# Kernel optimization log

Measured on AMD Instinct MI355X. Metric: run time of the kernel, lower is better.

Reference implementation:

```python
import jax, jax.numpy as jnp
import numpy as np
import math

ALPHA = math.exp(-0.001 * 1000.0)  # exp(-dt * tau_filter_inv)
T, B, D_IN, D_OUT = 2048, 32, 512, 512


def setup_inputs() -> dict:
    key = jax.random.key(0)
    k1, k2, k3 = jax.random.split(key, 3)
    bound = 1.0 / math.sqrt(D_IN)  # torch Linear default init range
    return {
        "input_tensor": jax.random.normal(k1, (T, B, D_IN), dtype=jnp.float32),
        "weight": jax.random.uniform(k2, (D_OUT, D_IN), minval=-bound, maxval=bound, dtype=jnp.float32),
        "bias": jax.random.uniform(k3, (D_OUT,), minval=-bound, maxval=bound, dtype=jnp.float32),
    }


def reference(input_tensor, weight, bias):
    # y[t] = W x[t] + b   -> [T, B, D_OUT]
    y = jnp.einsum("tbi,oi->tbo", input_tensor, weight) + bias
    alpha = jnp.asarray(ALPHA, dtype=y.dtype)

    # out[0] = y[0]; out[t] = alpha * out[t-1] + y[t]
    def step(carry, yt):
        out = alpha * carry + yt
        return out, out

    _, rest = jax.lax.scan(step, y[0], y[1:])
    return jnp.concatenate([y[:1], rest], axis=0)
```

## Files before the change

kernel.cpp:

```cpp
#include <hip/hip_runtime.h>
#include <stdint.h>

#define T_DIM 2048
#define B_DIM 32
#define DIN   512
#define DOUT  512
#define M_DIM (T_DIM * B_DIM)
#define COLS  (B_DIM * DIN)
#define COLS4 (COLS / 4)

#define ALPHA_F 0.36787944117144233f
#define INV_1MA 1.5819767068693265f

#define FT_T    32
#define FT_HALO 8
#define FT_ROWS (FT_T + FT_HALO)
#define FT_C4   32
#define FT_TT   (T_DIM / FT_T)
#define FT_CT   (COLS4 / FT_C4)

#define FCHUNKS  32
#define FCHUNK_T 64
#define FHALO    16

typedef float  floatx4 __attribute__((ext_vector_type(4)));
typedef __bf16 bf16x8  __attribute__((ext_vector_type(8)));

__device__ __forceinline__ uint32_t pk2(float a, float b) {
  uint32_t ua = __float_as_uint(a); ua += 0x7fffu + ((ua >> 16) & 1u);
  uint32_t ub = __float_as_uint(b); ub += 0x7fffu + ((ub >> 16) & 1u);
  return (ua >> 16) | (ub & 0xffff0000u);
}

__device__ __forceinline__ void gload_lds16(const void* g, void* lds) {
  __builtin_amdgcn_global_load_lds(
      (const __attribute__((address_space(1))) void*)g,
      (__attribute__((address_space(3))) void*)lds,
      16, 0, 0);
}

__device__ __forceinline__ void fma4(float4& c, const float4& v) {
  c.x = fmaf(ALPHA_F, c.x, v.x);
  c.y = fmaf(ALPHA_F, c.y, v.y);
  c.z = fmaf(ALPHA_F, c.z, v.z);
  c.w = fmaf(ALPHA_F, c.w, v.w);
}

__global__ void filter_x_kernel(const float* __restrict__ X,
                                uint16_t* __restrict__ XF,
                                const float* __restrict__ W,
                                uint16_t* __restrict__ WB)
{
  __shared__ __align__(16) float4 L4[FT_ROWS * FT_C4];

  if (blockIdx.y == FT_TT) {
    const int base = (blockIdx.x * 256 + threadIdx.x) * 8;
    const float4* W4 = (const float4*)W;
    float4 w0 = W4[base / 4];
    float4 w1 = W4[base / 4 + 1];
    uint4 p;
    p.x = pk2(w0.x, w0.y); p.y = pk2(w0.z, w0.w);
    p.z = pk2(w1.x, w1.y); p.w = pk2(w1.z, w1.w);
    *(uint4*)&WB[base] = p;
    return;
  }

  const int ct = blockIdx.x;
  const int tt = blockIdx.y;
  const int tid  = threadIdx.x;
  const int lane = tid & 63;
  const int w    = tid >> 6;
  const int t0   = tt * FT_T;
  const size_t gc4 = (size_t)ct * FT_C4;

  const int lrow = lane >> 5;
  const int lcol = lane & 31;

  if (tt == 0) {
    const float4 z = {0.0f, 0.0f, 0.0f, 0.0f};
    L4[tid] = z;
#pragma unroll
    for (int i = 0; i < 4; ++i) {
      const int row = 8 + (w * 4 + i) * 2;
      gload_lds16(X + ((size_t)(t0 + row - 8 + lrow) * COLS4 + gc4 + lcol) * 4,
                  &L4[row * FT_C4]);
    }
  } else {
#pragma unroll
    for (int i = 0; i < 5; ++i) {
      const int row = (w * 5 + i) * 2;
      gload_lds16(X + ((size_t)(t0 - 8 + row + lrow) * COLS4 + gc4 + lcol) * 4,
                  &L4[row * FT_C4]);
    }
  }
  __syncthreads();

  const int tg  = tid >> 5;
  const int col = tid & 31;
  float4 carry = {0.0f, 0.0f, 0.0f, 0.0f};
#pragma unroll
  for (int j = 0; j < 12; ++j) {
    float4 v = L4[(tg * 4 + j) * FT_C4 + col];
    fma4(carry, v);
    if (j >= 8) {
      const int o = tg * 4 + j - 8;
      uint2 p;
      p.x = pk2(carry.x, carry.y);
      p.y = pk2(carry.z, carry.w);
      *(uint2*)&XF[((size_t)(t0 + o) * COLS4 + gc4 + col) * 4] = p;
    }
  }
}

__launch_bounds__(256, 4)
__global__ void gemm_bf16_kernel(const uint16_t* __restrict__ XF,
                                 const uint16_t* __restrict__ WB,
                                 const float* __restrict__ bias,
                                 float* __restrict__ Y)
{
  __shared__ __align__(16) uint16_t As[128 * 64];
  __shared__ __align__(16) uint16_t Bs[128 * 64];

  const int bid = blockIdx.x;
  const int lg = (bid & 7) * 256 + (bid >> 3);
  const int n0 = (lg & 3) * 128;
  const int m0 = (lg >> 2) * 128;

  const int tid  = threadIdx.x;
  const int lane = tid & 63;
  const int w    = tid >> 6;
  const int r    = lane & 15;
  const int q    = lane >> 4;
  const int wm   = w >> 1;
  const int wn   = w & 1;

  const int srow_base = w * 32 + (lane >> 3);
  const int schunk    = lane & 7;

  floatx4 acc[4][4];
#pragma unroll
  for (int i = 0; i < 4; ++i)
#pragma unroll
    for (int j = 0; j < 4; ++j) {
      floatx4 z = {0.0f, 0.0f, 0.0f, 0.0f};
      acc[i][j] = z;
    }

  for (int kt = 0; kt < DIN / 64; ++kt) {
    const int k0 = kt * 64;
#pragma unroll
    for (int i = 0; i < 4; ++i) {
      const int row = srow_base + i * 8;
      const int sc = schunk ^ (row & 7);
      gload_lds16(XF + (size_t)(m0 + row) * DIN + k0 + sc * 8,
                  &As[(w * 32 + i * 8) * 64]);
      gload_lds16(WB + (size_t)(n0 + row) * DIN + k0 + sc * 8,
                  &Bs[(w * 32 + i * 8) * 64]);
    }
    __syncthreads();

#pragma unroll
    for (int kk = 0; kk < 2; ++kk) {
      bf16x8 af[4], bfr[4];
#pragma unroll
      for (int mi = 0; mi < 4; ++mi) {
        const int row = wm * 64 + mi * 16 + r;
        const int cch = (kk * 4 + q) ^ (row & 7);
        af[mi] = *(const bf16x8*)&As[row * 64 + (cch << 3)];
      }
#pragma unroll
      for (int ni = 0; ni < 4; ++ni) {
        const int row = wn * 64 + ni * 16 + r;
        const int cch = (kk * 4 + q) ^ (row & 7);
        bfr[ni] = *(const bf16x8*)&Bs[row * 64 + (cch << 3)];
      }
#pragma unroll
      for (int mi = 0; mi < 4; ++mi)
#pragma unroll
        for (int ni = 0; ni < 4; ++ni)
          acc[mi][ni] = __builtin_amdgcn_mfma_f32_16x16x32_bf16(
              af[mi], bfr[ni], acc[mi][ni], 0, 0, 0);
    }
    __syncthreads();
  }

#pragma unroll
  for (int mi = 0; mi < 4; ++mi) {
    const int rowb = m0 + wm * 64 + mi * 16;
    const int t = rowb >> 5;
    const float s = (1.0f - __expf(-(float)(t + 1))) * INV_1MA;
#pragma unroll
    for (int ni = 0; ni < 4; ++ni) {
      const int col = n0 + wn * 64 + ni * 16 + r;
      const float sb = s * bias[col];
#pragma unroll
      for (int j = 0; j < 4; ++j)
        Y[(size_t)(rowb + q * 4 + j) * DOUT + col] = acc[mi][ni][j] + sb;
    }
  }
}

__launch_bounds__(256, 2)
__global__ void gemm_bias_kernel(const float* __restrict__ X,
                                 const float* __restrict__ W,
                                 const float* __restrict__ bias,
                                 float* __restrict__ Y,
                                 float* __restrict__ halo,
                                 int halo_on)
{
  __shared__ __align__(16) uint16_t As[128 * 64];
  __shared__ __align__(16) uint16_t Bsh[128 * 64];

  const int tid  = threadIdx.x;
  const int lane = tid & 63;
  const int wave = tid >> 6;
  const int wm   = wave >> 1;
  const int wn   = wave & 1;
  const int r    = lane & 15;
  const int q    = lane >> 4;

  const int m0 = blockIdx.y * 128;
  const int n0 = blockIdx.x * 128;

  floatx4 acc[4][4];
#pragma unroll
  for (int i = 0; i < 4; ++i)
#pragma unroll
    for (int j = 0; j < 4; ++j) {
      floatx4 z = {0.0f, 0.0f, 0.0f, 0.0f};
      acc[i][j] = z;
    }

  for (int kt = 0; kt < DIN / 64; ++kt) {
    const int k0 = kt * 64;
#pragma unroll
    for (int j = 0; j < 4; ++j) {
      const int cid = tid + j * 256;
      const int row = cid >> 3;
      const int c   = cid & 7;
      const int slot = (c ^ (row & 7)) << 3;

      const float* ga = &X[(size_t)(m0 + row) * DIN + k0 + c * 8];
      float4 a0 = *(const float4*)ga;
      float4 a1 = *(const float4*)(ga + 4);
      uint4 pa;
      pa.x = pk2(a0.x, a0.y); pa.y = pk2(a0.z, a0.w);
      pa.z = pk2(a1.x, a1.y); pa.w = pk2(a1.z, a1.w);
      *(uint4*)&As[row * 64 + slot] = pa;

      const float* gb = &W[(size_t)(n0 + row) * DIN + k0 + c * 8];
      float4 b0 = *(const float4*)gb;
      float4 b1 = *(const float4*)(gb + 4);
      uint4 pb;
      pb.x = pk2(b0.x, b0.y); pb.y = pk2(b0.z, b0.w);
      pb.z = pk2(b1.x, b1.y); pb.w = pk2(b1.z, b1.w);
      *(uint4*)&Bsh[row * 64 + slot] = pb;
    }
    __syncthreads();

#pragma unroll
    for (int kk = 0; kk < 2; ++kk) {
      bf16x8 af[4], bfr[4];
#pragma unroll
      for (int mi = 0; mi < 4; ++mi) {
        const int row = wm * 64 + mi * 16 + r;
        const int c   = (kk * 4 + q) ^ (row & 7);
        af[mi] = *(const bf16x8*)&As[row * 64 + (c << 3)];
      }
#pragma unroll
      for (int ni = 0; ni < 4; ++ni) {
        const int row = wn * 64 + ni * 16 + r;
        const int c   = (kk * 4 + q) ^ (row & 7);
        bfr[ni] = *(const bf16x8*)&Bsh[row * 64 + (c << 3)];
      }
#pragma unroll
      for (int mi = 0; mi < 4; ++mi)
#pragma unroll
        for (int ni = 0; ni < 4; ++ni)
          acc[mi][ni] = __builtin_amdgcn_mfma_f32_16x16x32_bf16(
              af[mi], bfr[ni], acc[mi][ni], 0, 0, 0);
    }
    __syncthreads();
  }

#pragma unroll
  for (int ni = 0; ni < 4; ++ni) {
    const int col = n0 + wn * 64 + ni * 16 + r;
    const float bv = bias[col];
#pragma unroll
    for (int mi = 0; mi < 4; ++mi) {
      const int rowm = m0 + wm * 64 + mi * 16 + q * 4;
      const int t = rowm >> 5;
      const int b = rowm & 31;
      const int tloc = t & (FCHUNK_T - 1);
      const bool hw = halo_on && (tloc >= FCHUNK_T - FHALO) && (t < T_DIM - FCHUNK_T);
      const size_t hbase = hw
          ? ((size_t)(((t >> 6) + 1) * FHALO + (tloc - (FCHUNK_T - FHALO))) * COLS)
          : 0;
#pragma unroll
      for (int j = 0; j < 4; ++j) {
        const float v = acc[mi][ni][j] + bv;
        Y[(size_t)(rowm + j) * DOUT + col] = v;
        if (hw) halo[hbase + (size_t)(b + j) * DOUT + col] = v;
      }
    }
  }
}

__global__ void scan_kernel(float* __restrict__ Y,
                            const float* __restrict__ halo,
                            int chunk_len)
{
  const int col4 = blockIdx.x * blockDim.x + threadIdx.x;
  const int c = blockIdx.y;

  float4* Y4 = (float4*)Y;
  const float4* H4 = (const float4*)halo;

  float4 carry = {0.0f, 0.0f, 0.0f, 0.0f};
  if (c > 0) {
#pragma unroll
    for (int h = 0; h < FHALO; ++h) {
      float4 v = H4[(size_t)(c * FHALO + h) * COLS4 + col4];
      fma4(carry, v);
    }
  }

  size_t idx = (size_t)c * chunk_len * COLS4 + col4;
  float4 ynext = Y4[idx];
  for (int t = 0; t < chunk_len; ++t) {
    float4 y = ynext;
    if (t + 1 < chunk_len) ynext = Y4[idx + COLS4];
    fma4(carry, y);
    Y4[idx] = carry;
    idx += COLS4;
  }
}

extern "C" void kernel_launch(void* const* d_in, const int* in_sizes, int n_in,
                              void* d_out, int out_size, void* d_ws, size_t ws_size,
                              hipStream_t stream)
{
  const float* X    = (const float*)d_in[0];
  const float* W    = (const float*)d_in[1];
  const float* bias = (const float*)d_in[2];
  float* Y = (float*)d_out;

  const size_t need_new = (size_t)M_DIM * DIN * 2 + (size_t)DOUT * DIN * 2;

  if (ws_size >= need_new) {
    uint16_t* XF = (uint16_t*)d_ws;
    uint16_t* WB = XF + (size_t)M_DIM * DIN;

    dim3 gf(FT_CT, FT_TT + 1);
    filter_x_kernel<<<gf, 256, 0, stream>>>(X, XF, W, WB);
    gemm_bf16_kernel<<<2048, 256, 0, stream>>>(XF, WB, bias, Y);
  } else {
    float* halo = (float*)d_ws;
    const size_t halo_need = (size_t)FCHUNKS * FHALO * COLS * sizeof(float);
    const int halo_on = (ws_size >= halo_need) ? 1 : 0;

    dim3 g1(DOUT / 128, M_DIM / 128);
    gemm_bias_kernel<<<g1, 256, 0, stream>>>(X, W, bias, Y, halo, halo_on);

    const int n_chunks = halo_on ? FCHUNKS : 1;
    dim3 g2(COLS4 / 256, n_chunks);
    scan_kernel<<<g2, 256, 0, stream>>>(Y, halo, T_DIM / n_chunks);
  }
}
```

Measured before the change: 86.53 us.

## Replace bf16 GEMM with 256x256 tile, 4-stage async LDS pipeline

Swaps the 128x128 single-buffered bf16 GEMM for a 256x256-tile kernel with 512 threads. It uses a 4-deep ring of K=32 LDS buffers filled by global_load_lds, with explicit vmcnt waits and barriers. The aim is to overlap global loads with MFMA work and to raise arithmetic intensity per tile. In exchange it uses more registers (32 accumulators per wave) and launches only 512 blocks, which may leave load imbalance across CUs.

```diff
diff --git a/kernel.cpp b/kernel.cpp
--- a/kernel.cpp
+++ b/kernel.cpp
@@ -19,6 +19,9 @@
 #define FT_TT   (T_DIM / FT_T)
 #define FT_CT   (COLS4 / FT_C4)
 
+#define GBK  32
+#define NKT  (DIN / GBK)
+
 #define FCHUNKS  32
 #define FCHUNK_T 64
 #define FHALO    16
@@ -44,6 +47,16 @@
   c.y = fmaf(ALPHA_F, c.y, v.y);
   c.z = fmaf(ALPHA_F, c.z, v.z);
   c.w = fmaf(ALPHA_F, c.w, v.w);
+}
+
+__device__ __forceinline__ void waitcnt_vm(int n) {
+  switch (n) {
+    case 12: asm volatile("s_waitcnt vmcnt(12)" ::: "memory"); break;
+    case 8:  asm volatile("s_waitcnt vmcnt(8)"  ::: "memory"); break;
+    case 4:  asm volatile("s_waitcnt vmcnt(4)"  ::: "memory"); break;
+    default: asm volatile("s_waitcnt vmcnt(0)"  ::: "memory"); break;
+  }
+  __builtin_amdgcn_sched_barrier(0);
 }
 
 __global__ void filter_x_kernel(const float* __restrict__ X,
@@ -112,81 +125,94 @@
   }
 }
 
-__launch_bounds__(256, 4)
-__global__ void gemm_bf16_kernel(const uint16_t* __restrict__ XF,
-                                 const uint16_t* __restrict__ WB,
-                                 const float* __restrict__ bias,
-                                 float* __restrict__ Y)
-{
-  __shared__ __align__(16) uint16_t As[128 * 64];
-  __shared__ __align__(16) uint16_t Bs[128 * 64];
+__launch_bounds__(512, 2)
+__global__ void gemm_bf16_deep(const uint16_t* __restrict__ XF,
+                               const uint16_t* __restrict__ WB,
+                               const float* __restrict__ bias,
+                               float* __restrict__ Y)
+{
+  __shared__ __align__(16) uint16_t As[4][256 * GBK];
+  __shared__ __align__(16) uint16_t Bs[4][256 * GBK];
 
   const int bid = blockIdx.x;
-  const int lg = (bid & 7) * 256 + (bid >> 3);
-  const int n0 = (lg & 3) * 128;
-  const int m0 = (lg >> 2) * 128;
+  const int lg  = (bid & 7) * 64 + (bid >> 3);
+  const int n0  = (lg & 1) * 256;
+  const int m0  = (lg >> 1) * 256;
 
   const int tid  = threadIdx.x;
   const int lane = tid & 63;
   const int w    = tid >> 6;
+  const int wm   = w >> 2;
+  const int wn   = w & 3;
   const int r    = lane & 15;
   const int q    = lane >> 4;
-  const int wm   = w >> 1;
-  const int wn   = w & 1;
-
-  const int srow_base = w * 32 + (lane >> 3);
-  const int schunk    = lane & 7;
-
-  floatx4 acc[4][4];
-#pragma unroll
-  for (int i = 0; i < 4; ++i)
+
+
+#define STAGE(KT)                                                            \
+  {                                                                          \
+    const int b_ = (KT) & 3;                                                 \
+    _Pragma("unroll")                                                        \
+    for (int i = 0; i < 2; ++i) {                                            \
+      const int c   = tid + i * 512;                                         \
+      const int row = c >> 2;                                                \
+      const int lc  = (c & 3) ^ ((row >> 2) & 3);                            \
+      uint16_t* ldsA = (uint16_t*)&As[b_][(w * 64 + i * 512) * 8];           \
+      uint16_t* ldsB = (uint16_t*)&Bs[b_][(w * 64 + i * 512) * 8];           \
+      gload_lds16(XF + (size_t)(m0 + row) * DIN + (KT) * GBK + lc * 8, ldsA);\
+      gload_lds16(WB + (size_t)(n0 + row) * DIN + (KT) * GBK + lc * 8, ldsB);\
+    }                                                                        \
+  }
+
+  floatx4 acc[8][4];
+#pragma unroll
+  for (int i = 0; i < 8; ++i)
 #pragma unroll
     for (int j = 0; j < 4; ++j) {
       floatx4 z = {0.0f, 0.0f, 0.0f, 0.0f};
       acc[i][j] = z;
     }
 
-  for (int kt = 0; kt < DIN / 64; ++kt) {
-    const int k0 = kt * 64;
-#pragma unroll
-    for (int i = 0; i < 4; ++i) {
-      const int row = srow_base + i * 8;
-      const int sc = schunk ^ (row & 7);
-      gload_lds16(XF + (size_t)(m0 + row) * DIN + k0 + sc * 8,
-                  &As[(w * 32 + i * 8) * 64]);
-      gload_lds16(WB + (size_t)(n0 + row) * DIN + k0 + sc * 8,
-                  &Bs[(w * 32 + i * 8) * 64]);
-    }
-    __syncthreads();
-
-#pragma unroll
-    for (int kk = 0; kk < 2; ++kk) {
-      bf16x8 af[4], bfr[4];
-#pragma unroll
-      for (int mi = 0; mi < 4; ++mi) {
-        const int row = wm * 64 + mi * 16 + r;
-        const int cch = (kk * 4 + q) ^ (row & 7);
-        af[mi] = *(const bf16x8*)&As[row * 64 + (cch << 3)];
-      }
-#pragma unroll
-      for (int ni = 0; ni < 4; ++ni) {
-        const int row = wn * 64 + ni * 16 + r;
-        const int cch = (kk * 4 + q) ^ (row & 7);
-        bfr[ni] = *(const bf16x8*)&Bs[row * 64 + (cch << 3)];
-      }
-#pragma unroll
-      for (int mi = 0; mi < 4; ++mi)
-#pragma unroll
-        for (int ni = 0; ni < 4; ++ni)
-          acc[mi][ni] = __builtin_amdgcn_mfma_f32_16x16x32_bf16(
-              af[mi], bfr[ni], acc[mi][ni], 0, 0, 0);
-    }
-    __syncthreads();
-  }
-
-#pragma unroll
-  for (int mi = 0; mi < 4; ++mi) {
-    const int rowb = m0 + wm * 64 + mi * 16;
+  STAGE(0);
+  STAGE(1);
+  STAGE(2);
+
+  for (int kt = 0; kt < NKT; ++kt) {
+    if (kt + 3 < NKT) STAGE(kt + 3);
+
+    waitcnt_vm(kt < NKT - 3 ? 12 : 4 * (NKT - 1 - kt));
+    __builtin_amdgcn_s_barrier();
+    __builtin_amdgcn_sched_barrier(0);
+
+    const int b_ = kt & 3;
+    bf16x8 af[8], bfr[4];
+#pragma unroll
+    for (int mi = 0; mi < 8; ++mi) {
+      const int row  = wm * 128 + mi * 16 + r;
+      const int slot = q ^ ((row >> 2) & 3);
+      af[mi] = *(const bf16x8*)&As[b_][row * GBK + slot * 8];
+    }
+#pragma unroll
+    for (int ni = 0; ni < 4; ++ni) {
+      const int row  = wn * 64 + ni * 16 + r;
+      const int slot = q ^ ((row >> 2) & 3);
+      bfr[ni] = *(const bf16x8*)&Bs[b_][row * GBK + slot * 8];
+    }
+#pragma unroll
+    for (int mi = 0; mi < 8; ++mi)
+#pragma unroll
+      for (int ni = 0; ni < 4; ++ni)
+        acc[mi][ni] = __builtin_amdgcn_mfma_f32_16x16x32_bf16(
+            af[mi], bfr[ni], acc[mi][ni], 0, 0, 0);
+
+    asm volatile("s_waitcnt lgkmcnt(0)" ::: "memory");
+    __builtin_amdgcn_sched_barrier(0);
+    __builtin_amdgcn_s_barrier();
+  }
+#undef STAGE
+
+#pragma unroll
+  for (int mi = 0; mi < 8; ++mi) {
+    const int rowb = m0 + wm * 128 + mi * 16;
     const int t = rowb >> 5;
     const float s = (1.0f - __expf(-(float)(t + 1))) * INV_1MA;
 #pragma unroll
@@ -354,7 +380,7 @@
 
     dim3 gf(FT_CT, FT_TT + 1);
     filter_x_kernel<<<gf, 256, 0, stream>>>(X, XF, W, WB);
-    gemm_bf16_kernel<<<2048, 256, 0, stream>>>(XF, WB, bias, Y);
+    gemm_bf16_deep<<<512, 512, 0, stream>>>(XF, WB, bias, Y);
   } else {
     float* halo = (float*)d_ws;
     const size_t halo_need = (size_t)FCHUNKS * FHALO * COLS * sizeof(float);
```

Measured after the change: 104.8 us. 21.1% more time.
